# Performance work log

Hardware: AMD Instinct MI355X
Metric: run time of the kernel (lower is better)

The kernel has to match this reference:

```python
import jax, jax.numpy as jnp
import numpy as np

H = 256          # hidden_channels
R = 64           # num_rbf
N = 20000        # nodes
E = 320000       # edges
CUTOFF_LO = 0.0
CUTOFF_UP = 5.0
LN_EPS = 1e-5


def _layernorm(x, g, b):
    mu = jnp.mean(x, axis=-1, keepdims=True)
    var = jnp.var(x, axis=-1, keepdims=True)
    return (x - mu) * jax.lax.rsqrt(var + LN_EPS) * g + b


def _cosine_cutoff(r):
    # cutoff_lower == 0 branch of CosineCutoff
    c = 0.5 * (jnp.cos(r * (jnp.pi / CUTOFF_UP)) + 1.0)
    return c * (r < CUTOFF_UP).astype(r.dtype)


def setup_inputs() -> dict:
    key = jax.random.key(0)
    ks = jax.random.split(key, 16)
    def xavier(k, shape):
        fan_in, fan_out = shape[1], shape[0]
        lim = np.sqrt(6.0 / (fan_in + fan_out))
        return jax.random.uniform(k, shape, jnp.float32, -lim, lim)
    x = jax.random.normal(ks[0], (N, H), jnp.float32)
    edge_index = jax.random.randint(ks[1], (2, E), 0, N, jnp.int64)
    edge_weight = jax.random.uniform(ks[2], (E,), jnp.float32, 0.0, CUTOFF_UP)
    edge_attr = jax.random.normal(ks[3], (E, R), jnp.float32)
    return {
        "x": x,
        "edge_index": edge_index,
        "edge_weight": edge_weight,
        "edge_attr": edge_attr,
        "ln_g": jnp.ones((H,), jnp.float32),
        "ln_b": jnp.zeros((H,), jnp.float32),
        "Wq": xavier(ks[4], (H, H)), "bq": jnp.zeros((H,), jnp.float32),
        "Wk": xavier(ks[5], (H, H)), "bk": jnp.zeros((H,), jnp.float32),
        "Wv": xavier(ks[6], (H, H)), "bv": jnp.zeros((H,), jnp.float32),
        "Wo": xavier(ks[7], (H, H)), "bo": jnp.zeros((H,), jnp.float32),
        "Wdk": xavier(ks[8], (H, R)), "bdk": jnp.zeros((H,), jnp.float32),
        "Wdv": xavier(ks[9], (H, R)), "bdv": jnp.zeros((H,), jnp.float32),
    }


def reference(x, edge_index, edge_weight, edge_attr,
              ln_g, ln_b, Wq, bq, Wk, bk, Wv, bv, Wo, bo, Wdk, bdk, Wdv, bdv):
    src = edge_index[0]  # j (messages come from)
    dst = edge_index[1]  # i (messages aggregate to)

    x_norm = _layernorm(x, ln_g, ln_b)                     # [N,H]
    q = x_norm @ Wq.T + bq                                 # [N,H]
    k = x_norm @ Wk.T + bk
    v = x_norm @ Wv.T + bv

    dk = jax.nn.silu(edge_attr @ Wdk.T + bdk)              # [E,H]
    dv = jax.nn.silu(edge_attr @ Wdv.T + bdv)              # [E,H]

    q_i = q[dst]                                           # [E,H]
    k_j = k[src]
    v_j = v[src]

    attn = jnp.sum(q_i * k_j * dk, axis=1)                 # [E]
    attn = jax.nn.silu(attn) * _cosine_cutoff(edge_weight) # [E]

    msg = v_j * dv * attn[:, None]                         # [E,H]
    agg = jax.ops.segment_sum(msg, dst, num_segments=x.shape[0])  # [N,H]

    out = agg @ Wo.T + bo
    return x + out
```

## Files before the change

### kernel.cpp

```cpp
#include <hip/hip_runtime.h>
#include <math.h>

#define NN 20000
#define H 256
#define R 64
#define EE 320000
#define LN_EPS 1e-5f
#define NB 79

using short8  = __attribute__((ext_vector_type(8))) short;
using ushort8 = __attribute__((ext_vector_type(8))) unsigned short;
using f32x4   = __attribute__((ext_vector_type(4))) float;

typedef __attribute__((address_space(3))) unsigned int lds_uint;
typedef const __attribute__((address_space(1))) unsigned int glb_uint;

__device__ __forceinline__ float silu_f(float x) {
    return x * __builtin_amdgcn_rcpf(1.0f + __expf(-x));
}

__device__ __forceinline__ unsigned short f2bf(float f) {
    unsigned u = __float_as_uint(f);
    u += 0x7fff + ((u >> 16) & 1);
    return (unsigned short)(u >> 16);
}
__device__ __forceinline__ float bf2f(unsigned short s) {
    return __uint_as_float(((unsigned)s) << 16);
}
__device__ __forceinline__ unsigned short f2h(float f) {
    unsigned r;
    asm("v_cvt_f16_f32 %0, %1" : "=v"(r) : "v"(f));
    return (unsigned short)r;
}
__device__ __forceinline__ float h2f(unsigned short h) {
    float f;
    asm("v_cvt_f32_f16 %0, %1" : "=v"(f) : "v"((unsigned)h));
    return f;
}

__device__ __forceinline__ int sw_idx(int row, int col) {
    return row * 64 + ((((col >> 3) ^ (row & 7)) << 3) | (col & 7));
}
__device__ __forceinline__ int dh_idx(int row, int col) {
    return row * 128 + (col ^ (((row >> 2) & 3) << 4));
}

__global__ __launch_bounds__(256) void k_prep(
    const float* __restrict__ Wq, const float* __restrict__ Wk,
    const float* __restrict__ Wv, const float* __restrict__ Wo,
    const float* __restrict__ g,  const float* __restrict__ b,
    const float* __restrict__ bq, const float* __restrict__ bk, const float* __restrict__ bv,
    const float* __restrict__ Wdk, const float* __restrict__ Wdv,
    unsigned short* __restrict__ wqkv_p, unsigned short* __restrict__ wo_p,
    unsigned short* __restrict__ wdk_p,  unsigned short* __restrict__ wdv_p,
    float* __restrict__ bias3, int* __restrict__ hist)
{
    const int bid = blockIdx.x, t = threadIdx.x;
    if (bid < 128) {
        const int mat = bid >> 5;
        const float* W = mat == 0 ? Wq : (mat == 1 ? Wk : (mat == 2 ? Wv : Wo));
        unsigned short* out = (mat < 3) ? wqkv_p + (size_t)mat * 131072 : wo_p;
        const int fold = mat < 3;
        const int flat = (bid & 31) * 256 + t;
        const int tile = flat >> 9;
        const int rem  = flat & 511;
        const int ks   = rem >> 6;
        const int lane = rem & 63;
        const int nl = lane & 15, quad = lane >> 4;
        const int h  = tile * 16 + nl;
        const int c0 = ks * 32 + quad * 8;
        short8 hi8, lo8;
        #pragma unroll
        for (int j = 0; j < 8; ++j) {
            float wv = W[(size_t)h * 256 + c0 + j];
            if (fold) wv *= g[c0 + j];
            const unsigned short hh = f2bf(wv);
            hi8[j] = (short)hh;
            lo8[j] = (short)f2bf(wv - bf2f(hh));
        }
        unsigned short* ob = out + ((size_t)(tile * 8 + ks)) * 1024;
        *(short8*)&ob[lane * 8] = hi8;
        *(short8*)&ob[512 + lane * 8] = lo8;
    } else if (bid < 160) {
        const int flat = (bid - 128) * 256 + t;
        const int mat  = flat >> 12;
        const int rem  = flat & 4095;
        const int hh   = rem >> 11;
        const int r2   = rem & 2047;
        const int row  = r2 >> 4;
        const int col4 = (r2 & 15) * 4;
        const float* W = mat == 0 ? Wdk : Wdv;
        unsigned short* out = (mat == 0 ? wdk_p : wdv_p) + hh * 16384;
        const float4 w4 = *(const float4*)(W + (size_t)(hh * 128 + row) * 64 + col4);
        const unsigned short h0 = f2bf(w4.x), h1 = f2bf(w4.y), h2 = f2bf(w4.z), h3 = f2bf(w4.w);
        ushort4 hi4 = {h0, h1, h2, h3};
        ushort4 lo4 = {f2bf(w4.x - bf2f(h0)), f2bf(w4.y - bf2f(h1)),
                       f2bf(w4.z - bf2f(h2)), f2bf(w4.w - bf2f(h3))};
        const int di = sw_idx(row, col4);
        *(ushort4*)&out[di] = hi4;
        *(ushort4*)&out[8192 + di] = lo4;
    } else if (bid < 163) {
        const int mat = bid - 160, h = t;
        const float* W  = mat == 0 ? Wq : (mat == 1 ? Wk : Wv);
        const float* bb = mat == 0 ? bq : (mat == 1 ? bk : bv);
        float s = 0.f;
        const float* wr = W + (size_t)h * 256;
        for (int c = 0; c < 256; c += 4) {
            const float4 w4 = *(const float4*)(wr + c);
            const float4 b4 = *(const float4*)(b + c);
            s += w4.x * b4.x + w4.y * b4.y + w4.z * b4.z + w4.w * b4.w;
        }
        bias3[mat * 256 + h] = bb[h] + s;
    } else {
        const int i = (bid - 163) * 256 + t;
        if (i < NN) hist[i] = 0;
    }
}

__global__ __launch_bounds__(64, 2) void k_ln_qkv(
    const float* __restrict__ x,
    const unsigned short* __restrict__ wqkv_p, const float* __restrict__ bias3,
    float* __restrict__ q, float* __restrict__ k, float* __restrict__ v)
{
    const int t = threadIdx.x;
    const int lane = t & 63;
    const int nl = lane & 15, quad = lane >> 4;
    const int nbase = blockIdx.x * 16;
    const int node = nbase + nl;
    const bool nv = node < NN;

    float xv[64];
    float sum = 0.f, sq = 0.f;
    {
        const float* xp = x + (size_t)node * H + quad * 8;
        #pragma unroll
        for (int ks = 0; ks < 8; ++ks) {
            float4 x0 = {0.f,0.f,0.f,0.f}, x1 = {0.f,0.f,0.f,0.f};
            if (nv) {
                x0 = *(const float4*)(xp + ks * 32);
                x1 = *(const float4*)(xp + ks * 32 + 4);
            }
            xv[ks*8+0]=x0.x; xv[ks*8+1]=x0.y; xv[ks*8+2]=x0.z; xv[ks*8+3]=x0.w;
            xv[ks*8+4]=x1.x; xv[ks*8+5]=x1.y; xv[ks*8+6]=x1.z; xv[ks*8+7]=x1.w;
            sum += x0.x+x0.y+x0.z+x0.w + x1.x+x1.y+x1.z+x1.w;
            sq  += x0.x*x0.x+x0.y*x0.y+x0.z*x0.z+x0.w*x0.w
                 + x1.x*x1.x+x1.y*x1.y+x1.z*x1.z+x1.w*x1.w;
        }
    }
    sum += __shfl_xor(sum, 16); sum += __shfl_xor(sum, 32);
    sq  += __shfl_xor(sq, 16);  sq  += __shfl_xor(sq, 32);
    const float mu  = sum * (1.0f / H);
    const float var = sq * (1.0f / H) - mu * mu;
    const float rs  = rsqrtf(var + LN_EPS);

    short8 a_hi[8], a_lo[8];
    #pragma unroll
    for (int ks = 0; ks < 8; ++ks) {
        #pragma unroll
        for (int j = 0; j < 8; ++j) {
            const float z = (xv[ks*8+j] - mu) * rs;
            const unsigned short hh = f2bf(z);
            a_hi[ks][j] = (short)hh;
            a_lo[ks][j] = (short)f2bf(z - bf2f(hh));
        }
    }

    for (int mat = 0; mat < 3; ++mat) {
        float* outp = mat == 0 ? q : (mat == 1 ? k : v);
        const float* bp = bias3 + mat * 256;
        const unsigned short* wb = wqkv_p + (size_t)mat * 131072 + lane * 8;
        for (int tile = 0; tile < 16; ++tile) {
            const unsigned short* gb = wb + (size_t)tile * 8192;
            const float bbv = bp[tile * 16 + nl];
            f32x4 acc = {bbv, bbv, bbv, bbv};
            #pragma unroll
            for (int ks = 0; ks < 8; ++ks) {
                const short8 b_hi = *(const short8*)(gb + ks * 1024);
                const short8 b_lo = *(const short8*)(gb + ks * 1024 + 512);
                acc = __builtin_amdgcn_mfma_f32_16x16x32_bf16(a_hi[ks], b_hi, acc, 0, 0, 0);
                acc = __builtin_amdgcn_mfma_f32_16x16x32_bf16(a_lo[ks], b_hi, acc, 0, 0, 0);
                acc = __builtin_amdgcn_mfma_f32_16x16x32_bf16(a_hi[ks], b_lo, acc, 0, 0, 0);
            }
            #pragma unroll
            for (int r = 0; r < 4; ++r) {
                const int onode = nbase + quad * 4 + r;
                if (onode < NN)
                    outp[(size_t)onode * H + tile * 16 + nl] = acc[r];
            }
        }
    }
}

__global__ __launch_bounds__(256) void k_hist(const int* __restrict__ ei, int* __restrict__ hist) {
    int e = blockIdx.x * 256 + threadIdx.x;
    if (e < EE) atomicAdd(&hist[ei[EE + e]], 1);
}

__global__ __launch_bounds__(256) void k_scan1(const int* __restrict__ hist,
                                               int* __restrict__ cursor, int* __restrict__ bsum) {
    const int t = threadIdx.x, i = blockIdx.x * 256 + t;
    const int lane = t & 63, w = t >> 6;
    const int v = (i < NN) ? hist[i] : 0;
    int incl = v;
    #pragma unroll
    for (int off = 1; off < 64; off <<= 1) {
        int u = __shfl_up(incl, off);
        if (lane >= off) incl += u;
    }
    __shared__ int ws[4];
    if (lane == 63) ws[w] = incl;
    __syncthreads();
    int base = 0;
    #pragma unroll
    for (int j = 0; j < 4; ++j) if (j < w) base += ws[j];
    if (i < NN) cursor[i] = base + incl - v;
    if (t == 255) bsum[blockIdx.x] = base + incl;
}

__global__ __launch_bounds__(128) void k_scan2(int* __restrict__ bsum) {
    __shared__ int buf[128];
    const int t = threadIdx.x;
    const int v = (t < NB) ? bsum[t] : 0;
    buf[t] = v;
    __syncthreads();
    #pragma unroll
    for (int off = 1; off < 128; off <<= 1) {
        int add = (t >= off) ? buf[t - off] : 0;
        __syncthreads();
        buf[t] += add;
        __syncthreads();
    }
    if (t < NB) bsum[t] = buf[t] - v;
}

__global__ __launch_bounds__(256) void k_scatter(const int* __restrict__ ei,
                                                 int* __restrict__ cursor,
                                                 const int* __restrict__ bsum,
                                                 int* __restrict__ perm) {
    int e = blockIdx.x * 256 + threadIdx.x;
    if (e < EE) {
        int d = ei[EE + e];
        int pos = atomicAdd(&cursor[d], 1) + bsum[d >> 8];
        perm[pos] = e;
    }
}

__global__ __launch_bounds__(256, 3) void k_edge(
    const float* __restrict__ q, const float* __restrict__ k, const float* __restrict__ v,
    const int* __restrict__ ei, const float* __restrict__ ew, const float* __restrict__ ea,
    const unsigned short* __restrict__ wdk_p, const float* __restrict__ bdk,
    const unsigned short* __restrict__ wdv_p, const float* __restrict__ bdv,
    const int* __restrict__ perm,
    float* __restrict__ agg)
{
    __shared__ __align__(16) unsigned short w_region[2 * 128 * 64];
    __shared__ __align__(16) unsigned short dks_h[64 * 128];
    __shared__ float attn_s[64];
    __shared__ int src_s[64], dst_s[64];

    const unsigned short* w_hi_s = w_region;
    const unsigned short* w_lo_s = w_region + 128 * 64;

    const int t    = threadIdx.x;
    const int bi   = blockIdx.x;
    const int eb   = ((bi & 7) * 625 + (bi >> 3)) * 64;
    const int lane = t & 63, wave = t >> 6;
    const int nl   = lane & 15, quad = lane >> 4;
    const int estrip = wave * 16;
    const int tx = t & 31, ty = t >> 5;
    const int h0 = tx * 4, e0 = ty * 8;

    {
        const ushort8* sp = (const ushort8*)wdk_p + t;
        ushort8* dpw = (ushort8*)w_region + (t & 192);
        #pragma unroll
        for (int c = 0; c < 8; ++c)
            __builtin_amdgcn_global_load_lds((glb_uint*)(sp + c * 256),
                                             (lds_uint*)(dpw + c * 256), 16, 0, 0);
    }

    if (t < 64) {
        const int e = perm[eb + t];
        src_s[t] = ei[e];
        dst_s[t] = ei[EE + e];
        attn_s[t] = 0.f;
    }

    short8 a_hi[2], a_lo[2];
    {
        const int e = perm[eb + estrip + nl];
        const float* ap = ea + (size_t)e * R + quad * 8;
        #pragma unroll
        for (int ks = 0; ks < 2; ++ks) {
            const float4 x0 = *(const float4*)(ap + ks * 32);
            const float4 x1 = *(const float4*)(ap + ks * 32 + 4);
            const float zz[8] = {x0.x, x0.y, x0.z, x0.w, x1.x, x1.y, x1.z, x1.w};
            #pragma unroll
            for (int j = 0; j < 8; ++j) {
                const unsigned short hv = f2bf(zz[j]);
                a_hi[ks][j] = (short)hv;
                a_lo[ks][j] = (short)f2bf(zz[j] - bf2f(hv));
            }
        }
    }
    __syncthreads();

    for (int img = 0; img < 4; ++img) {
        const int hh = img & 1;

        if (img == 2 && t < 64) {
            const int e = perm[eb + t];
            const float rr = ew[e];
            const float cut = (rr < 5.0f) ? 0.5f * (__cosf(rr * 0.6283185307f) + 1.0f) : 0.0f;
            attn_s[t] = silu_f(attn_s[t]) * cut;
        }

        const float* bias = (img < 2) ? bdk : bdv;
        f32x4 accA[8];
        #pragma unroll
        for (int tt = 0; tt < 8; ++tt) {
            const int wrow = tt * 16 + nl;
            short8 b_hi[2], b_lo[2];
            #pragma unroll
            for (int ks = 0; ks < 2; ++ks) {
                const int idx = wrow * 64 + ((((ks * 4 + quad) ^ (nl & 7)) << 3));
                b_hi[ks] = *(const short8*)&w_hi_s[idx];
                b_lo[ks] = *(const short8*)&w_lo_s[idx];
            }
            const float bb = bias[hh * 128 + tt * 16 + nl];
            f32x4 acc = {bb, bb, bb, bb};
            #pragma unroll
            for (int ks = 0; ks < 2; ++ks) {
                acc = __builtin_amdgcn_mfma_f32_16x16x32_bf16(a_hi[ks], b_hi[ks], acc, 0, 0, 0);
                acc = __builtin_amdgcn_mfma_f32_16x16x32_bf16(a_lo[ks], b_hi[ks], acc, 0, 0, 0);
                acc = __builtin_amdgcn_mfma_f32_16x16x32_bf16(a_hi[ks], b_lo[ks], acc, 0, 0, 0);
            }
            accA[tt] = acc;
        }
        __syncthreads();

        if (img < 3) {
            const unsigned short* nip = (img == 0) ? wdk_p + 16384
                                      : (img == 1) ? wdv_p : wdv_p + 16384;
            const ushort8* sp = (const ushort8*)nip + t;
            ushort8* dpw = (ushort8*)w_region + (t & 192);
            #pragma unroll
            for (int c = 0; c < 8; ++c)
                __builtin_amdgcn_global_load_lds((glb_uint*)(sp + c * 256),
                                                 (lds_uint*)(dpw + c * 256), 16, 0, 0);
        }

        #pragma unroll
        for (int tt = 0; tt < 8; ++tt)
            #pragma unroll
            for (int r = 0; r < 4; ++r)
                dks_h[dh_idx(estrip + quad * 4 + r, tt * 16 + nl)] =
                    f2h(silu_f(accA[tt][r]));

        if (img < 2) {
            #pragma unroll
            for (int i = 0; i < 8; ++i) {
                const int d = dst_s[e0 + i], s = src_s[e0 + i];
                const float4 qi = *(const float4*)(q + (size_t)d * H + hh * 128 + h0);
                const float4 kj = *(const float4*)(k + (size_t)s * H + hh * 128 + h0);
                const ushort4 dk4 = *(const ushort4*)&dks_h[dh_idx(e0 + i, h0)];
                float part = qi.x * kj.x * h2f(dk4.x) + qi.y * kj.y * h2f(dk4.y)
                           + qi.z * kj.z * h2f(dk4.z) + qi.w * kj.w * h2f(dk4.w);
                #pragma unroll
                for (int off = 16; off; off >>= 1) part += __shfl_xor(part, off);
                if (tx == 0) attn_s[e0 + i] += part;
            }
        } else {
            float4 m = {0.f, 0.f, 0.f, 0.f};
            int cur_d = -1;
            #pragma unroll
            for (int i = 0; i < 8; ++i) {
                const int d = dst_s[e0 + i], s = src_s[e0 + i];
                const float a = attn_s[e0 + i];
                const float4 vj = *(const float4*)(v + (size_t)s * H + hh * 128 + h0);
                const ushort4 dv4 = *(const ushort4*)&dks_h[dh_idx(e0 + i, h0)];
                float4 mi;
                mi.x = vj.x * h2f(dv4.x) * a;
                mi.y = vj.y * h2f(dv4.y) * a;
                mi.z = vj.z * h2f(dv4.z) * a;
                mi.w = vj.w * h2f(dv4.w) * a;
                if (d != cur_d) {
                    if (cur_d >= 0) {
                        float* dp = agg + (size_t)cur_d * H + hh * 128 + h0;
                        atomicAdd(dp + 0, m.x); atomicAdd(dp + 1, m.y);
                        atomicAdd(dp + 2, m.z); atomicAdd(dp + 3, m.w);
                    }
                    m = mi; cur_d = d;
                } else {
                    m.x += mi.x; m.y += mi.y; m.z += mi.z; m.w += mi.w;
                }
            }
            {
                float* dp = agg + (size_t)cur_d * H + hh * 128 + h0;
                atomicAdd(dp + 0, m.x); atomicAdd(dp + 1, m.y);
                atomicAdd(dp + 2, m.z); atomicAdd(dp + 3, m.w);
            }
        }
        __syncthreads();
    }
}

__global__ __launch_bounds__(64, 2) void k_out(
    const float* __restrict__ aggm, const unsigned short* __restrict__ wo_p,
    const float* __restrict__ bo, const float* __restrict__ x, float* __restrict__ out)
{
    const int t = threadIdx.x;
    const int lane = t & 63;
    const int nl = lane & 15, quad = lane >> 4;
    const int nbase = blockIdx.x * 16;
    const int node = nbase + nl;
    const bool nv = node < NN;

    short8 a_hi[8], a_lo[8];
    {
        const float* ap = aggm + (size_t)node * H + quad * 8;
        #pragma unroll
        for (int ks = 0; ks < 8; ++ks) {
            float4 x0 = {0.f,0.f,0.f,0.f}, x1 = {0.f,0.f,0.f,0.f};
            if (nv) { x0 = *(const float4*)(ap + ks * 32); x1 = *(const float4*)(ap + ks * 32 + 4); }
            const float zz[8] = {x0.x,x0.y,x0.z,x0.w,x1.x,x1.y,x1.z,x1.w};
            #pragma unroll
            for (int j = 0; j < 8; ++j) {
                const unsigned short hh = f2bf(zz[j]);
                a_hi[ks][j] = (short)hh;
                a_lo[ks][j] = (short)f2bf(zz[j] - bf2f(hh));
            }
        }
    }
    for (int tile = 0; tile < 16; ++tile) {
        const unsigned short* gb = wo_p + (size_t)tile * 8192 + lane * 8;
        const float bbv = bo[tile * 16 + nl];
        f32x4 acc = {bbv, bbv, bbv, bbv};
        #pragma unroll
        for (int ks = 0; ks < 8; ++ks) {
            const short8 b_hi = *(const short8*)(gb + ks * 1024);
            const short8 b_lo = *(const short8*)(gb + ks * 1024 + 512);
            acc = __builtin_amdgcn_mfma_f32_16x16x32_bf16(a_hi[ks], b_hi, acc, 0, 0, 0);
            acc = __builtin_amdgcn_mfma_f32_16x16x32_bf16(a_lo[ks], b_hi, acc, 0, 0, 0);
            acc = __builtin_amdgcn_mfma_f32_16x16x32_bf16(a_hi[ks], b_lo, acc, 0, 0, 0);
        }
        #pragma unroll
        for (int r = 0; r < 4; ++r) {
            const int onode = nbase + quad * 4 + r;
            if (onode < NN) {
                const size_t oi = (size_t)onode * H + tile * 16 + nl;
                out[oi] = x[oi] + acc[r];
            }
        }
    }
}

extern "C" void kernel_launch(void* const* d_in, const int* in_sizes, int n_in,
                              void* d_out, int out_size, void* d_ws, size_t ws_size,
                              hipStream_t stream) {
    const float* x   = (const float*)d_in[0];
    const int*   ei  = (const int*)d_in[1];
    const float* ew  = (const float*)d_in[2];
    const float* ea  = (const float*)d_in[3];
    const float* g   = (const float*)d_in[4];
    const float* b   = (const float*)d_in[5];
    const float* Wq  = (const float*)d_in[6];  const float* bq  = (const float*)d_in[7];
    const float* Wk  = (const float*)d_in[8];  const float* bk  = (const float*)d_in[9];
    const float* Wv  = (const float*)d_in[10]; const float* bv  = (const float*)d_in[11];
    const float* Wo  = (const float*)d_in[12]; const float* bo  = (const float*)d_in[13];
    const float* Wdk = (const float*)d_in[14]; const float* bdk = (const float*)d_in[15];
    const float* Wdv = (const float*)d_in[16]; const float* bdv = (const float*)d_in[17];

    float* q    = (float*)d_ws;
    float* k    = q + (size_t)NN * H;
    float* v    = k + (size_t)NN * H;
    float* agg  = v + (size_t)NN * H;
    int*   hist = (int*)(agg + (size_t)NN * H);
    int*   cur  = hist + NN;
    int*   bsum = cur + NN;
    int*   perm = bsum + 128;
    unsigned short* wqkv_p = (unsigned short*)(perm + EE);
    unsigned short* wo_p   = wqkv_p + 393216;
    unsigned short* wdk_p  = wo_p + 131072;
    unsigned short* wdv_p  = wdk_p + 32768;
    float* bias3 = (float*)(wdv_p + 32768);

    hipMemsetAsync(agg, 0, (size_t)NN * H * sizeof(float), stream);
    k_prep<<<242, 256, 0, stream>>>(Wq, Wk, Wv, Wo, g, b, bq, bk, bv, Wdk, Wdv,
                                    wqkv_p, wo_p, wdk_p, wdv_p, bias3, hist);
    k_hist<<<EE / 256, 256, 0, stream>>>(ei, hist);
    k_ln_qkv<<<(NN + 15) / 16, 64, 0, stream>>>(x, wqkv_p, bias3, q, k, v);
    k_scan1<<<NB, 256, 0, stream>>>(hist, cur, bsum);
    k_scan2<<<1, 128, 0, stream>>>(bsum);
    k_scatter<<<EE / 256, 256, 0, stream>>>(ei, cur, bsum, perm);
    k_edge<<<EE / 64, 256, 0, stream>>>(q, k, v, ei, ew, ea, wdk_p, bdk, wdv_p, bdv, perm, agg);
    k_out<<<(NN + 15) / 16, 64, 0, stream>>>(agg, wo_p, bo, x, (float*)d_out);
}
```

Baseline: 647.8 us.

## Process two node tiles per wave in QKV/out GEMMs and restructure edge aggregation

The LN+QKV and output projection kernels now handle 32 nodes per wave, so each loaded weight fragment feeds two MFMA accumulators and weight traffic per node halves. The edge kernel reuses the q row when consecutive sorted edges share a destination. Message aggregation now gives each thread one channel over 32 consecutive edges, accumulating in a register and issuing atomics only when the destination changes. The edge kernel's occupancy hint drops from 3 to 2 blocks, and the wider tiles raise register pressure.

```diff
diff --git a/kernel.cpp b/kernel.cpp
--- a/kernel.cpp
+++ b/kernel.cpp
@@ -125,13 +125,15 @@
     const int t = threadIdx.x;
     const int lane = t & 63;
     const int nl = lane & 15, quad = lane >> 4;
-    const int nbase = blockIdx.x * 16;
-    const int node = nbase + nl;
-    const bool nv = node < NN;
-
-    float xv[64];
-    float sum = 0.f, sq = 0.f;
-    {
+    const int nbase = blockIdx.x * 32;
+
+    short8 a_hi[2][8], a_lo[2][8];
+    #pragma unroll
+    for (int s = 0; s < 2; ++s) {
+        const int node = nbase + s * 16 + nl;
+        const bool nv = node < NN;
+        float xv[64];
+        float sum = 0.f, sq = 0.f;
         const float* xp = x + (size_t)node * H + quad * 8;
         #pragma unroll
         for (int ks = 0; ks < 8; ++ks) {
@@ -146,22 +148,20 @@
             sq  += x0.x*x0.x+x0.y*x0.y+x0.z*x0.z+x0.w*x0.w
                  + x1.x*x1.x+x1.y*x1.y+x1.z*x1.z+x1.w*x1.w;
         }
-    }
-    sum += __shfl_xor(sum, 16); sum += __shfl_xor(sum, 32);
-    sq  += __shfl_xor(sq, 16);  sq  += __shfl_xor(sq, 32);
-    const float mu  = sum * (1.0f / H);
-    const float var = sq * (1.0f / H) - mu * mu;
-    const float rs  = rsqrtf(var + LN_EPS);
-
-    short8 a_hi[8], a_lo[8];
-    #pragma unroll
-    for (int ks = 0; ks < 8; ++ks) {
-        #pragma unroll
-        for (int j = 0; j < 8; ++j) {
-            const float z = (xv[ks*8+j] - mu) * rs;
-            const unsigned short hh = f2bf(z);
-            a_hi[ks][j] = (short)hh;
-            a_lo[ks][j] = (short)f2bf(z - bf2f(hh));
+        sum += __shfl_xor(sum, 16); sum += __shfl_xor(sum, 32);
+        sq  += __shfl_xor(sq, 16);  sq  += __shfl_xor(sq, 32);
+        const float mu  = sum * (1.0f / H);
+        const float var = sq * (1.0f / H) - mu * mu;
+        const float rs  = rsqrtf(var + LN_EPS);
+        #pragma unroll
+        for (int ks = 0; ks < 8; ++ks) {
+            #pragma unroll
+            for (int j = 0; j < 8; ++j) {
+                const float z = (xv[ks*8+j] - mu) * rs;
+                const unsigned short hh = f2bf(z);
+                a_hi[s][ks][j] = (short)hh;
+                a_lo[s][ks][j] = (short)f2bf(z - bf2f(hh));
+            }
         }
     }
 
@@ -172,20 +172,25 @@
         for (int tile = 0; tile < 16; ++tile) {
             const unsigned short* gb = wb + (size_t)tile * 8192;
             const float bbv = bp[tile * 16 + nl];
-            f32x4 acc = {bbv, bbv, bbv, bbv};
+            f32x4 acc0 = {bbv, bbv, bbv, bbv};
+            f32x4 acc1 = {bbv, bbv, bbv, bbv};
             #pragma unroll
             for (int ks = 0; ks < 8; ++ks) {
                 const short8 b_hi = *(const short8*)(gb + ks * 1024);
                 const short8 b_lo = *(const short8*)(gb + ks * 1024 + 512);
-                acc = __builtin_amdgcn_mfma_f32_16x16x32_bf16(a_hi[ks], b_hi, acc, 0, 0, 0);
-                acc = __builtin_amdgcn_mfma_f32_16x16x32_bf16(a_lo[ks], b_hi, acc, 0, 0, 0);
-                acc = __builtin_amdgcn_mfma_f32_16x16x32_bf16(a_hi[ks], b_lo, acc, 0, 0, 0);
+                acc0 = __builtin_amdgcn_mfma_f32_16x16x32_bf16(a_hi[0][ks], b_hi, acc0, 0, 0, 0);
+                acc0 = __builtin_amdgcn_mfma_f32_16x16x32_bf16(a_lo[0][ks], b_hi, acc0, 0, 0, 0);
+                acc0 = __builtin_amdgcn_mfma_f32_16x16x32_bf16(a_hi[0][ks], b_lo, acc0, 0, 0, 0);
+                acc1 = __builtin_amdgcn_mfma_f32_16x16x32_bf16(a_hi[1][ks], b_hi, acc1, 0, 0, 0);
+                acc1 = __builtin_amdgcn_mfma_f32_16x16x32_bf16(a_lo[1][ks], b_hi, acc1, 0, 0, 0);
+                acc1 = __builtin_amdgcn_mfma_f32_16x16x32_bf16(a_hi[1][ks], b_lo, acc1, 0, 0, 0);
             }
             #pragma unroll
             for (int r = 0; r < 4; ++r) {
-                const int onode = nbase + quad * 4 + r;
-                if (onode < NN)
-                    outp[(size_t)onode * H + tile * 16 + nl] = acc[r];
+                const int on0 = nbase + quad * 4 + r;
+                const int on1 = nbase + 16 + quad * 4 + r;
+                if (on0 < NN) outp[(size_t)on0 * H + tile * 16 + nl] = acc0[r];
+                if (on1 < NN) outp[(size_t)on1 * H + tile * 16 + nl] = acc1[r];
             }
         }
     }
@@ -245,7 +250,7 @@
     }
 }
 
-__global__ __launch_bounds__(256, 3) void k_edge(
+__global__ __launch_bounds__(256, 2) void k_edge(
     const float* __restrict__ q, const float* __restrict__ k, const float* __restrict__ v,
     const int* __restrict__ ei, const float* __restrict__ ew, const float* __restrict__ ea,
     const unsigned short* __restrict__ wdk_p, const float* __restrict__ bdk,
@@ -292,9 +297,9 @@
         const float* ap = ea + (size_t)e * R + quad * 8;
         #pragma unroll
         for (int ks = 0; ks < 2; ++ks) {
-            const float4 x0 = *(const float4*)(ap + ks * 32);
-            const float4 x1 = *(const float4*)(ap + ks * 32 + 4);
-            const float zz[8] = {x0.x, x0.y, x0.z, x0.w, x1.x, x1.y, x1.z, x1.w};
+            const f32x4 x0 = *(const f32x4*)(ap + ks * 32);
+            const f32x4 x1 = *(const f32x4*)(ap + ks * 32 + 4);
+            const float zz[8] = {x0[0], x0[1], x0[2], x0[3], x1[0], x1[1], x1[2], x1[3]};
             #pragma unroll
             for (int j = 0; j < 8; ++j) {
                 const unsigned short hv = f2bf(zz[j]);
@@ -358,10 +363,15 @@
                     f2h(silu_f(accA[tt][r]));
 
         if (img < 2) {
+            float4 qi = {0.f, 0.f, 0.f, 0.f};
+            int pd = -1;
             #pragma unroll
             for (int i = 0; i < 8; ++i) {
                 const int d = dst_s[e0 + i], s = src_s[e0 + i];
-                const float4 qi = *(const float4*)(q + (size_t)d * H + hh * 128 + h0);
+                if (d != pd) {
+                    qi = *(const float4*)(q + (size_t)d * H + hh * 128 + h0);
+                    pd = d;
+                }
                 const float4 kj = *(const float4*)(k + (size_t)s * H + hh * 128 + h0);
                 const ushort4 dk4 = *(const ushort4*)&dks_h[dh_idx(e0 + i, h0)];
                 float part = qi.x * kj.x * h2f(dk4.x) + qi.y * kj.y * h2f(dk4.y)
@@ -371,35 +381,23 @@
                 if (tx == 0) attn_s[e0 + i] += part;
             }
         } else {
-            float4 m = {0.f, 0.f, 0.f, 0.f};
-            int cur_d = -1;
-            #pragma unroll
-            for (int i = 0; i < 8; ++i) {
-                const int d = dst_s[e0 + i], s = src_s[e0 + i];
-                const float a = attn_s[e0 + i];
-                const float4 vj = *(const float4*)(v + (size_t)s * H + hh * 128 + h0);
-                const ushort4 dv4 = *(const ushort4*)&dks_h[dh_idx(e0 + i, h0)];
-                float4 mi;
-                mi.x = vj.x * h2f(dv4.x) * a;
-                mi.y = vj.y * h2f(dv4.y) * a;
-                mi.z = vj.z * h2f(dv4.z) * a;
-                mi.w = vj.w * h2f(dv4.w) * a;
+            __syncthreads();
+            const int c    = t & 127;
+            const int ebas = (t >> 7) * 32;
+            float accf = 0.f;
+            int cur_d = dst_s[ebas];
+            #pragma unroll 8
+            for (int e2 = 0; e2 < 32; ++e2) {
+                const int e = ebas + e2;
+                const int d = dst_s[e];
                 if (d != cur_d) {
-                    if (cur_d >= 0) {
-                        float* dp = agg + (size_t)cur_d * H + hh * 128 + h0;
-                        atomicAdd(dp + 0, m.x); atomicAdd(dp + 1, m.y);
-                        atomicAdd(dp + 2, m.z); atomicAdd(dp + 3, m.w);
-                    }
-                    m = mi; cur_d = d;
-                } else {
-                    m.x += mi.x; m.y += mi.y; m.z += mi.z; m.w += mi.w;
+                    atomicAdd(&agg[(size_t)cur_d * H + hh * 128 + c], accf);
+                    accf = 0.f; cur_d = d;
                 }
-            }
-            {
-                float* dp = agg + (size_t)cur_d * H + hh * 128 + h0;
-                atomicAdd(dp + 0, m.x); atomicAdd(dp + 1, m.y);
-                atomicAdd(dp + 2, m.z); atomicAdd(dp + 3, m.w);
-            }
+                const float vv = v[(size_t)src_s[e] * H + hh * 128 + c];
+                accf += vv * h2f(dks_h[dh_idx(e, c)]) * attn_s[e];
+            }
+            atomicAdd(&agg[(size_t)cur_d * H + hh * 128 + c], accf);
         }
         __syncthreads();
     }
@@ -412,12 +410,13 @@
     const int t = threadIdx.x;
     const int lane = t & 63;
     const int nl = lane & 15, quad = lane >> 4;
-    const int nbase = blockIdx.x * 16;
-    const int node = nbase + nl;
-    const bool nv = node < NN;
-
-    short8 a_hi[8], a_lo[8];
-    {
+    const int nbase = blockIdx.x * 32;
+
+    short8 a_hi[2][8], a_lo[2][8];
+    #pragma unroll
+    for (int s = 0; s < 2; ++s) {
+        const int node = nbase + s * 16 + nl;
+        const bool nv = node < NN;
         const float* ap = aggm + (size_t)node * H + quad * 8;
         #pragma unroll
         for (int ks = 0; ks < 8; ++ks) {
@@ -427,29 +426,38 @@
             #pragma unroll
             for (int j = 0; j < 8; ++j) {
                 const unsigned short hh = f2bf(zz[j]);
-                a_hi[ks][j] = (short)hh;
-                a_lo[ks][j] = (short)f2bf(zz[j] - bf2f(hh));
+                a_hi[s][ks][j] = (short)hh;
+                a_lo[s][ks][j] = (short)f2bf(zz[j] - bf2f(hh));
             }
         }
     }
     for (int tile = 0; tile < 16; ++tile) {
         const unsigned short* gb = wo_p + (size_t)tile * 8192 + lane * 8;
         const float bbv = bo[tile * 16 + nl];
-        f32x4 acc = {bbv, bbv, bbv, bbv};
+        f32x4 acc0 = {bbv, bbv, bbv, bbv};
+        f32x4 acc1 = {bbv, bbv, bbv, bbv};
         #pragma unroll
         for (int ks = 0; ks < 8; ++ks) {
             const short8 b_hi = *(const short8*)(gb + ks * 1024);
             const short8 b_lo = *(const short8*)(gb + ks * 1024 + 512);
-            acc = __builtin_amdgcn_mfma_f32_16x16x32_bf16(a_hi[ks], b_hi, acc, 0, 0, 0);
-            acc = __builtin_amdgcn_mfma_f32_16x16x32_bf16(a_lo[ks], b_hi, acc, 0, 0, 0);
-            acc = __builtin_amdgcn_mfma_f32_16x16x32_bf16(a_hi[ks], b_lo, acc, 0, 0, 0);
+            acc0 = __builtin_amdgcn_mfma_f32_16x16x32_bf16(a_hi[0][ks], b_hi, acc0, 0, 0, 0);
+            acc0 = __builtin_amdgcn_mfma_f32_16x16x32_bf16(a_lo[0][ks], b_hi, acc0, 0, 0, 0);
+            acc0 = __builtin_amdgcn_mfma_f32_16x16x32_bf16(a_hi[0][ks], b_lo, acc0, 0, 0, 0);
+            acc1 = __builtin_amdgcn_mfma_f32_16x16x32_bf16(a_hi[1][ks], b_hi, acc1, 0, 0, 0);
+            acc1 = __builtin_amdgcn_mfma_f32_16x16x32_bf16(a_lo[1][ks], b_hi, acc1, 0, 0, 0);
+            acc1 = __builtin_amdgcn_mfma_f32_16x16x32_bf16(a_hi[1][ks], b_lo, acc1, 0, 0, 0);
         }
         #pragma unroll
         for (int r = 0; r < 4; ++r) {
-            const int onode = nbase + quad * 4 + r;
-            if (onode < NN) {
-                const size_t oi = (size_t)onode * H + tile * 16 + nl;
-                out[oi] = x[oi] + acc[r];
+            const int on0 = nbase + quad * 4 + r;
+            const int on1 = nbase + 16 + quad * 4 + r;
+            if (on0 < NN) {
+                const size_t oi = (size_t)on0 * H + tile * 16 + nl;
+                out[oi] = x[oi] + acc0[r];
+            }
+            if (on1 < NN) {
+                const size_t oi = (size_t)on1 * H + tile * 16 + nl;
+                out[oi] = x[oi] + acc1[r];
             }
         }
     }
@@ -489,10 +497,10 @@
     k_prep<<<242, 256, 0, stream>>>(Wq, Wk, Wv, Wo, g, b, bq, bk, bv, Wdk, Wdv,
                                     wqkv_p, wo_p, wdk_p, wdv_p, bias3, hist);
     k_hist<<<EE / 256, 256, 0, stream>>>(ei, hist);
-    k_ln_qkv<<<(NN + 15) / 16, 64, 0, stream>>>(x, wqkv_p, bias3, q, k, v);
+    k_ln_qkv<<<(NN + 31) / 32, 64, 0, stream>>>(x, wqkv_p, bias3, q, k, v);
     k_scan1<<<NB, 256, 0, stream>>>(hist, cur, bsum);
     k_scan2<<<1, 128, 0, stream>>>(bsum);
     k_scatter<<<EE / 256, 256, 0, stream>>>(ei, cur, bsum, perm);
     k_edge<<<EE / 64, 256, 0, stream>>>(q, k, v, ei, ew, ea, wdk_p, bdk, wdv_p, bdv, perm, agg);
-    k_out<<<(NN + 15) / 16, 64, 0, stream>>>(agg, wo_p, bo, x, (float*)d_out);
-}
+    k_out<<<(NN + 31) / 32, 64, 0, stream>>>(agg, wo_p, bo, x, (float*)d_out);
+}
```

Result: slower. 715.2 us (+10.4%).
